# Optimization experiments

Hardware: AMD Instinct MI355X
Metric: run time of the kernel (lower is better)

Reference implementation:

```python
import jax, jax.numpy as jnp
import numpy as np

B, S = 1, 128            # batch, timesteps
N_LGN = 17400            # LGN input units (dense_shape[1])
N_POST = 50000           # V1 neurons (dense_shape[0])
NNZ = 800000             # number of synapses
N_BASIS = 5              # synaptic receptor basis functions
N_RECEPT = 10            # receptor types


def setup_inputs() -> dict:
    key = jax.random.key(0)
    k1, k2, k3, k4, k5, k6 = jax.random.split(key, 6)
    inp = jax.random.normal(k1, (B, S, N_LGN), dtype=jnp.float32)
    rows = jax.random.randint(k2, (NNZ,), 0, N_POST)
    cols = jax.random.randint(k3, (NNZ,), 0, N_LGN)
    indices = jnp.stack([rows, cols], axis=1)  # [nnz, 2] sparse coords
    weights = jax.random.normal(k4, (NNZ,), dtype=jnp.float32)
    synaptic_weights = jax.random.uniform(k5, (N_RECEPT, N_BASIS), dtype=jnp.float32)
    syn_ids = jax.random.randint(k6, (NNZ,), 0, N_RECEPT)
    return {
        "inp": inp,
        "indices": indices,
        "weights": weights,
        "synaptic_weights": synaptic_weights,
        "syn_ids": syn_ids,
        "n_neurons": N_POST,
    }


def reference(inp, indices, weights, synaptic_weights, syn_ids, n_neurons):
    b, s, n_lgn = inp.shape
    x = inp.reshape(b * s, n_lgn)               # [Bt, n_lgn], Bt = batch*time
    rows = indices[:, 0]                        # post-synaptic neuron id
    cols = indices[:, 1]                        # pre-synaptic LGN id
    factors = synaptic_weights[syn_ids]         # [nnz, n_basis] (tf.gather)
    xg = x.T[cols]                              # [nnz, Bt] gathered presyn activity
    n_basis = factors.shape[1]
    outs = []
    for r in range(n_basis):                    # small fixed loop over receptor bases
        vals = weights * factors[:, r]          # per-receptor sparse values
        # sparse_dense_matmul(sparse_w_in, inp, adjoint_b=True) == scatter-add over rows
        outs.append(jax.ops.segment_sum(xg * vals[:, None], rows, num_segments=n_neurons))
    i_in = jnp.stack(outs)                      # [n_basis, n_post, Bt]
    out = jnp.transpose(i_in, (2, 1, 0))        # [Bt, n_post, n_basis]
    return out.reshape(b, s, -1)                # [batch, time, n_post*n_basis]
```

## Files before the change

kernel.cpp:

```cpp
#include <hip/hip_runtime.h>
#include <hip/hip_bf16.h>
#include <stdint.h>

#define N_LGN   17400
#define N_POST  50000
#define NNZ     800000
#define N_BASIS 5
#define ELL_CAP 48

#define NBKT      196
#define CAPB      5120
#define BIN_CHUNK 4096
#define BIN_BLOCKS ((NNZ + BIN_CHUNK - 1) / BIN_CHUNK)

#define TPOSE_CBLK   32
#define TPOSE_BLOCKS ((N_LGN + TPOSE_CBLK - 1) / TPOSE_CBLK)

__global__ __launch_bounds__(256) void k_prep(const float* __restrict__ inp,
                                              __hip_bfloat162* __restrict__ xTb,
                                              const int2* __restrict__ idx2,
                                              const float* __restrict__ w,
                                              const int* __restrict__ syn,
                                              int* __restrict__ bucketCnt,
                                              int2* __restrict__ bEdges) {
    __shared__ alignas(16) int2 ebuf[BIN_CHUNK];
    __shared__ unsigned char sbuf[BIN_CHUNK];
    __shared__ int hcnt[256], hstart[256], hcur[256], gbase[256];
    int tid = threadIdx.x;
    if (blockIdx.x < BIN_BLOCKS) {
        int base = blockIdx.x * BIN_CHUNK;
        int ne = NNZ - base; if (ne > BIN_CHUNK) ne = BIN_CHUNK;
        hcnt[tid] = 0;
        __syncthreads();
        int2 pk[16]; int bk[16];
#pragma unroll
        for (int i = 0; i < 16; ++i) {
            int p = i * 256 + tid;
            bk[i] = -1;
            if (p < ne) {
                int2 rc = idx2[base + p];
                float wv = w[base + p];
                int sy = syn[base + p];
                int b  = rc.x >> 8;
                int rl = rc.x & 255;
                pk[i] = make_int2(rc.y | (sy << 15) | (rl << 19), __float_as_int(wv));
                bk[i] = b;
                atomicAdd(&hcnt[b], 1);
            }
        }
        __syncthreads();
        int v = hcnt[tid];
        hstart[tid] = v;
        __syncthreads();
        for (int off = 1; off < 256; off <<= 1) {
            int t = (tid >= off) ? hstart[tid - off] : 0;
            __syncthreads();
            hstart[tid] += t;
            __syncthreads();
        }
        int excl = hstart[tid] - v;
        hstart[tid] = excl;
        hcur[tid]  = excl;
        if (tid < NBKT) gbase[tid] = atomicAdd(&bucketCnt[tid], v);
        __syncthreads();
#pragma unroll
        for (int i = 0; i < 16; ++i) {
            if (bk[i] >= 0) {
                int pos = atomicAdd(&hcur[bk[i]], 1);
                ebuf[pos] = pk[i];
                sbuf[pos] = (unsigned char)bk[i];
            }
        }
        __syncthreads();
        for (int p = tid; p < ne; p += 256) {
            int b  = sbuf[p];
            int gi = gbase[b] + (p - hstart[b]);
            if (gi < CAPB) bEdges[b * CAPB + gi] = ebuf[p];
        }
    } else {
        float* tile = (float*)ebuf;
        int c0 = (blockIdx.x - BIN_BLOCKS) * TPOSE_CBLK;
        for (int it = 0; it < 16; ++it) {
            int flat = it * 256 + tid;
            int s  = flat >> 5;
            int cl = flat & 31;
            int c  = c0 + cl;
            float v = 0.0f;
            if (c < N_LGN) v = inp[s * N_LGN + c];
            tile[cl * 129 + s] = v;
        }
        __syncthreads();
        for (int it = 0; it < 8; ++it) {
            int flat = it * 256 + tid;
            int cl = flat >> 6;
            int sp = flat & 63;
            int c  = c0 + cl;
            if (c < N_LGN) {
                float2 f = make_float2(tile[cl * 129 + 2 * sp], tile[cl * 129 + 2 * sp + 1]);
                xTb[c * 64 + sp] = __float22bfloat162_rn(f);
            }
        }
    }
}

__global__ __launch_bounds__(512) void k_build(const int2* __restrict__ bEdges,
                                               const int* __restrict__ bucketCnt,
                                               int2* __restrict__ ell,
                                               int* __restrict__ counts) {
    __shared__ alignas(16) int2 slab[256 * ELL_CAP];
    __shared__ int rcnt[256];
    int tid = threadIdx.x;
    int b   = blockIdx.x;
    if (tid < 256) rcnt[tid] = 0;
    __syncthreads();
    int cnt = bucketCnt[b]; if (cnt > CAPB) cnt = CAPB;
    for (int p = tid; p < cnt; p += 512) {
        int2 e = bEdges[b * CAPB + p];
        int rl = (e.x >> 19) & 0xFF;
        int r = atomicAdd(&rcnt[rl], 1);
        if (r < ELL_CAP)
            slab[rl * ELL_CAP + r] =
                make_int2((e.x & 0x7FFF) | (((e.x >> 15) & 0xF) << 16), e.y);
    }
    __syncthreads();
    const int4* s4 = (const int4*)slab;
    int4* e4 = (int4*)(ell + (size_t)b * (256 * ELL_CAP));
    for (int i = tid; i < 256 * ELL_CAP / 2; i += 512) e4[i] = s4[i];
    if (tid < 256) {
        int row = b * 256 + tid;
        if (row < N_POST) counts[row] = rcnt[tid];
    }
}

__global__ __launch_bounds__(256) void k_transpose_bf16(const float* __restrict__ inp,
                                                        __hip_bfloat162* __restrict__ xTb) {
    __shared__ float tile[64 * 129];
    int c0  = blockIdx.x * 64;
    int tid = threadIdx.x;
    for (int it = 0; it < 32; ++it) {
        int flat = it * 256 + tid;
        int s  = flat >> 6;
        int cl = flat & 63;
        int c  = c0 + cl;
        float v = 0.0f;
        if (c < N_LGN) v = inp[s * N_LGN + c];
        tile[cl * 129 + s] = v;
    }
    __syncthreads();
    for (int it = 0; it < 16; ++it) {
        int flat = it * 256 + tid;
        int cl = flat >> 6;
        int sp = flat & 63;
        int c  = c0 + cl;
        if (c < N_LGN) {
            float2 f = make_float2(tile[cl * 129 + 2 * sp], tile[cl * 129 + 2 * sp + 1]);
            xTb[c * 64 + sp] = __float22bfloat162_rn(f);
        }
    }
}

__global__ __launch_bounds__(256) void k_hist(const int4* __restrict__ idx2,
                                              int* __restrict__ counts) {
    int t = blockIdx.x * 256 + threadIdx.x;
    if (t >= NNZ / 2) return;
    int4 rc = idx2[t];
    atomicAdd(&counts[rc.x], 1);
    atomicAdd(&counts[rc.z], 1);
}

__global__ __launch_bounds__(1024) void k_scan1(const int* __restrict__ counts,
                                                int* __restrict__ rowStart,
                                                int* __restrict__ blockSums) {
    __shared__ int tmp[1024];
    int tid = threadIdx.x;
    int gid = blockIdx.x * 1024 + tid;
    int v = (gid < N_POST) ? counts[gid] : 0;
    tmp[tid] = v;
    __syncthreads();
    for (int off = 1; off < 1024; off <<= 1) {
        int t = (tid >= off) ? tmp[tid - off] : 0;
        __syncthreads();
        tmp[tid] += t;
        __syncthreads();
    }
    if (gid < N_POST) rowStart[gid] = tmp[tid] - v;
    if (tid == 1023) blockSums[blockIdx.x] = tmp[1023];
}

__global__ __launch_bounds__(64) void k_scan2(const int* __restrict__ blockSums,
                                              int* __restrict__ blockOffsets, int nblk) {
    __shared__ int tmp[64];
    int tid = threadIdx.x;
    int v = (tid < nblk) ? blockSums[tid] : 0;
    tmp[tid] = v;
    __syncthreads();
    for (int off = 1; off < 64; off <<= 1) {
        int t = (tid >= off) ? tmp[tid - off] : 0;
        __syncthreads();
        tmp[tid] += t;
        __syncthreads();
    }
    if (tid < nblk) blockOffsets[tid] = tmp[tid] - v;
}

__global__ __launch_bounds__(1024) void k_scan3(int* __restrict__ rowStart,
                                                const int* __restrict__ blockOffsets) {
    int gid = blockIdx.x * 1024 + threadIdx.x;
    if (gid < N_POST) rowStart[gid] += blockOffsets[blockIdx.x];
}

__global__ __launch_bounds__(256) void k_scatter_csr(const int4* __restrict__ idx2,
                                                     const float2* __restrict__ w2,
                                                     const int2* __restrict__ syn2,
                                                     const int* __restrict__ rowStart,
                                                     int* __restrict__ cursor,
                                                     int2* __restrict__ edges) {
    int t = blockIdx.x * 256 + threadIdx.x;
    if (t >= NNZ / 2) return;
    int4 rc = idx2[t];
    float2 ww = w2[t];
    int2 sy = syn2[t];
    int p0 = rowStart[rc.x] + atomicAdd(&cursor[rc.x], 1);
    edges[p0] = make_int2(rc.y | (sy.x << 16), __float_as_int(ww.x));
    int p1 = rowStart[rc.z] + atomicAdd(&cursor[rc.z], 1);
    edges[p1] = make_int2(rc.w | (sy.y << 16), __float_as_int(ww.y));
}

#define EDGE_FMA(XW, FA, F4)                                          \
    a0[0] = fmaf((XW).x, (FA).x, a0[0]); a1[0] = fmaf((XW).y, (FA).x, a1[0]); \
    a0[1] = fmaf((XW).x, (FA).y, a0[1]); a1[1] = fmaf((XW).y, (FA).y, a1[1]); \
    a0[2] = fmaf((XW).x, (FA).z, a0[2]); a1[2] = fmaf((XW).y, (FA).z, a1[2]); \
    a0[3] = fmaf((XW).x, (FA).w, a0[3]); a1[3] = fmaf((XW).y, (FA).w, a1[3]); \
    a0[4] = fmaf((XW).x, (F4),   a0[4]); a1[4] = fmaf((XW).y, (F4),   a1[4]);

__global__ __launch_bounds__(512, 8) void k_compute(const __hip_bfloat162* __restrict__ xTb,
                                                    const int2* __restrict__ edges,
                                                    const int* __restrict__ rowStart,
                                                    const int* __restrict__ counts,
                                                    const float* __restrict__ sw,
                                                    float2* __restrict__ out2,
                                                    int cap, int useEll) {
    __shared__ alignas(16) float facsP[80];
    __shared__ float accLds[40 * 133];
    __shared__ alignas(16) int2 eLds[8 * ELL_CAP];
    int tid  = threadIdx.x;
    int wave = tid >> 6;
    int lane = tid & 63;
    int n    = blockIdx.x * 8 + wave;
    int cnt  = counts[n];
    if (cnt > cap) cnt = cap;

    if (tid < 50) facsP[(tid / 5) * 8 + (tid % 5)] = sw[tid];
    if (useEll && tid < 8 * ELL_CAP / 2) {
        ((int4*)eLds)[tid] =
            ((const int4*)(edges + (size_t)blockIdx.x * (8 * ELL_CAP)))[tid];
    }
    __syncthreads();

    float a0[N_BASIS] = {0.f, 0.f, 0.f, 0.f, 0.f};
    float a1[N_BASIS] = {0.f, 0.f, 0.f, 0.f, 0.f};

    if (useEll) {
        const int4* ep4 = (const int4*)(eLds + wave * ELL_CAP);
        int j = 0;
        for (; j + 3 < cnt; j += 4) {
            int4 E0 = ep4[(j >> 1)];
            int4 E1 = ep4[(j >> 1) + 1];
            int c0 = E0.x & 0xFFFF, sy0 = E0.x >> 16; float w0 = __int_as_float(E0.y);
            int c1 = E0.z & 0xFFFF, sy1 = E0.z >> 16; float w1 = __int_as_float(E0.w);
            int c2 = E1.x & 0xFFFF, sy2 = E1.x >> 16; float w2 = __int_as_float(E1.y);
            int c3 = E1.z & 0xFFFF, sy3 = E1.z >> 16; float w3 = __int_as_float(E1.w);
            float2 x0 = __bfloat1622float2(xTb[c0 * 64 + lane]);
            float2 x1 = __bfloat1622float2(xTb[c1 * 64 + lane]);
            float2 x2 = __bfloat1622float2(xTb[c2 * 64 + lane]);
            float2 x3 = __bfloat1622float2(xTb[c3 * 64 + lane]);
            float4 fA0 = *(const float4*)&facsP[sy0 * 8]; float f40 = facsP[sy0 * 8 + 4];
            float4 fA1 = *(const float4*)&facsP[sy1 * 8]; float f41 = facsP[sy1 * 8 + 4];
            float4 fA2 = *(const float4*)&facsP[sy2 * 8]; float f42 = facsP[sy2 * 8 + 4];
            float4 fA3 = *(const float4*)&facsP[sy3 * 8]; float f43 = facsP[sy3 * 8 + 4];
            float2 xw0 = make_float2(x0.x * w0, x0.y * w0);
            float2 xw1 = make_float2(x1.x * w1, x1.y * w1);
            float2 xw2 = make_float2(x2.x * w2, x2.y * w2);
            float2 xw3 = make_float2(x3.x * w3, x3.y * w3);
            EDGE_FMA(xw0, fA0, f40)
            EDGE_FMA(xw1, fA1, f41)
            EDGE_FMA(xw2, fA2, f42)
            EDGE_FMA(xw3, fA3, f43)
        }
        for (; j < cnt; ++j) {
            int2 e = eLds[wave * ELL_CAP + j];
            int c = e.x & 0xFFFF, sy = e.x >> 16;
            float w = __int_as_float(e.y);
            float2 x = __bfloat1622float2(xTb[c * 64 + lane]);
            float4 fA = *(const float4*)&facsP[sy * 8]; float f4 = facsP[sy * 8 + 4];
            float2 xw = make_float2(x.x * w, x.y * w);
            EDGE_FMA(xw, fA, f4)
        }
    } else {
        const int2* ep = edges + rowStart[n];
        int j = 0;
        for (; j + 1 < cnt; j += 2) {
            int2 e0 = ep[j];
            int2 e1 = ep[j + 1];
            int c0 = e0.x & 0xFFFF, sy0 = e0.x >> 16;
            int c1 = e1.x & 0xFFFF, sy1 = e1.x >> 16;
            float2 x0 = __bfloat1622float2(xTb[c0 * 64 + lane]);
            float2 x1 = __bfloat1622float2(xTb[c1 * 64 + lane]);
            float w0 = __int_as_float(e0.y);
            float w1 = __int_as_float(e1.y);
            float4 fA0 = *(const float4*)&facsP[sy0 * 8]; float f40 = facsP[sy0 * 8 + 4];
            float4 fA1 = *(const float4*)&facsP[sy1 * 8]; float f41 = facsP[sy1 * 8 + 4];
            float2 xw0 = make_float2(x0.x * w0, x0.y * w0);
            float2 xw1 = make_float2(x1.x * w1, x1.y * w1);
            EDGE_FMA(xw0, fA0, f40)
            EDGE_FMA(xw1, fA1, f41)
        }
        if (j < cnt) {
            int2 e0 = ep[j];
            int c0 = e0.x & 0xFFFF, sy0 = e0.x >> 16;
            float2 x0 = __bfloat1622float2(xTb[c0 * 64 + lane]);
            float w0 = __int_as_float(e0.y);
            float4 fA0 = *(const float4*)&facsP[sy0 * 8]; float f40 = facsP[sy0 * 8 + 4];
            float2 xw0 = make_float2(x0.x * w0, x0.y * w0);
            EDGE_FMA(xw0, fA0, f40)
        }
    }

#pragma unroll
    for (int r = 0; r < N_BASIS; ++r) {
        int jj = wave * 5 + r;
        accLds[jj * 133 + 2 * lane]     = a0[r];
        accLds[jj * 133 + 2 * lane + 1] = a1[r];
    }
    __syncthreads();

    int base2 = blockIdx.x * 20;
    for (int it = 0; it < 5; ++it) {
        int flat = it * 512 + tid;
        int s  = flat / 20;
        int jj = flat % 20;
        float f0 = accLds[(2 * jj) * 133 + s];
        float f1 = accLds[(2 * jj + 1) * 133 + s];
        out2[s * 125000 + base2 + jj] = make_float2(f0, f1);
    }
}

extern "C" void kernel_launch(void* const* d_in, const int* in_sizes, int n_in,
                              void* d_out, int out_size, void* d_ws, size_t ws_size,
                              hipStream_t stream) {
    const float* inp     = (const float*)d_in[0];
    const int*   indices = (const int*)d_in[1];
    const float* weights = (const float*)d_in[2];
    const float* sw      = (const float*)d_in[3];
    const int*   syn     = (const int*)d_in[4];

    char* ws = (char*)d_ws;
    __hip_bfloat162* xTb = (__hip_bfloat162*)(ws);
    int* counts          = (int*)(ws + 4454400);

    const size_t ELL_BYTES_END = 4654400ULL + (size_t)N_POST * ELL_CAP * 8;
    bool useEll = (ws_size >= ELL_BYTES_END);

    if (useEll) {
        int2* ell = (int2*)(ws + 4654400);
        int2* bEdges   = (int2*)d_out;
        int*  bucketCnt = (int*)((char*)d_out + (size_t)NBKT * CAPB * 8);
        hipMemsetAsync(bucketCnt, 0, 1024, stream);
        k_prep<<<BIN_BLOCKS + TPOSE_BLOCKS, 256, 0, stream>>>(
            inp, xTb, (const int2*)indices, weights, syn, bucketCnt, bEdges);
        k_build<<<NBKT, 512, 0, stream>>>(bEdges, bucketCnt, ell, counts);
        k_compute<<<N_POST / 8, 512, 0, stream>>>(xTb, ell, nullptr, counts, sw,
                                                  (float2*)d_out, ELL_CAP, 1);
    } else {
        int* cursor    = (int*)(ws + 4654400);
        int* rowStart  = (int*)(ws + 4854400);
        int* blockSums = (int*)(ws + 5054400);
        int* blockOffs = (int*)(ws + 5054656);
        int2* edges    = (int2*)(ws + 5054912);
        hipMemsetAsync(counts, 0, 400000, stream);
        k_transpose_bf16<<<(N_LGN + 63) / 64, 256, 0, stream>>>(inp, xTb);
        k_hist<<<(NNZ / 2 + 255) / 256, 256, 0, stream>>>((const int4*)indices, counts);
        k_scan1<<<(N_POST + 1023) / 1024, 1024, 0, stream>>>(counts, rowStart, blockSums);
        k_scan2<<<1, 64, 0, stream>>>(blockSums, blockOffs, (N_POST + 1023) / 1024);
        k_scan3<<<(N_POST + 1023) / 1024, 1024, 0, stream>>>(rowStart, blockOffs);
        k_scatter_csr<<<(NNZ / 2 + 255) / 256, 256, 0, stream>>>(
            (const int4*)indices, (const float2*)weights, (const int2*)syn,
            rowStart, cursor, edges);
        k_compute<<<N_POST / 8, 512, 0, stream>>>(xTb, edges, rowStart, counts, sw,
                                                  (float2*)d_out, 1 << 30, 0);
    }
}
```

Before: 214.7 us.

## Process two ELL rows per wave with zero-padded slabs to remove tail loops

Adds a dedicated ELL compute kernel in which each wave handles two neurons and walks both rows together in steps of four. Eight independent gathers are in flight per iteration instead of four. The build kernel now zero-fills the ELL slab, so padded entries contribute zero and the per-row tail loop can be dropped; iterations run to the longer of the two rows. The cost is more registers (launch bounds lowered to 6), extra work on padding entries, and an extra LDS zeroing pass in the build kernel.

Measured after the change: 205.8 us. 4.1% less time.

```diff
diff --git a/kernel.cpp b/kernel.cpp
--- a/kernel.cpp
+++ b/kernel.cpp
@@ -112,6 +112,10 @@
     int tid = threadIdx.x;
     int b   = blockIdx.x;
     if (tid < 256) rcnt[tid] = 0;
+    {
+        int4* s4w = (int4*)slab;
+        for (int i = tid; i < 256 * ELL_CAP / 2; i += 512) s4w[i] = make_int4(0, 0, 0, 0);
+    }
     __syncthreads();
     int cnt = bucketCnt[b]; if (cnt > CAPB) cnt = CAPB;
     for (int p = tid; p < cnt; p += 512) {
@@ -226,104 +230,147 @@
     edges[p1] = make_int2(rc.w | (sy.y << 16), __float_as_int(ww.y));
 }
 
-#define EDGE_FMA(XW, FA, F4)                                          \
-    a0[0] = fmaf((XW).x, (FA).x, a0[0]); a1[0] = fmaf((XW).y, (FA).x, a1[0]); \
-    a0[1] = fmaf((XW).x, (FA).y, a0[1]); a1[1] = fmaf((XW).y, (FA).y, a1[1]); \
-    a0[2] = fmaf((XW).x, (FA).z, a0[2]); a1[2] = fmaf((XW).y, (FA).z, a1[2]); \
-    a0[3] = fmaf((XW).x, (FA).w, a0[3]); a1[3] = fmaf((XW).y, (FA).w, a1[3]); \
-    a0[4] = fmaf((XW).x, (F4),   a0[4]); a1[4] = fmaf((XW).y, (F4),   a1[4]);
+#define EDGE_FMA2(P0, P1, XW, FA, F4)                                             \
+    P0[0] = fmaf((XW).x, (FA).x, P0[0]); P1[0] = fmaf((XW).y, (FA).x, P1[0]);     \
+    P0[1] = fmaf((XW).x, (FA).y, P0[1]); P1[1] = fmaf((XW).y, (FA).y, P1[1]);     \
+    P0[2] = fmaf((XW).x, (FA).z, P0[2]); P1[2] = fmaf((XW).y, (FA).z, P1[2]);     \
+    P0[3] = fmaf((XW).x, (FA).w, P0[3]); P1[3] = fmaf((XW).y, (FA).w, P1[3]);     \
+    P0[4] = fmaf((XW).x, (F4),   P0[4]); P1[4] = fmaf((XW).y, (F4),   P1[4]);
+
+#define DECODE_GATHER(EX, EY, XW, FA, F4)                                         \
+    {                                                                             \
+        int c_  = (EX) & 0xFFFF; int sy_ = (EX) >> 16;                            \
+        float2 x_ = __bfloat1622float2(xTb[c_ * 64 + lane]);                      \
+        float w_  = __int_as_float(EY);                                           \
+        FA = *(const float4*)&facsP[sy_ * 8]; F4 = facsP[sy_ * 8 + 4];            \
+        XW = make_float2(x_.x * w_, x_.y * w_);                                   \
+    }
+
+__global__ __launch_bounds__(512, 6) void k_compute_ell(const __hip_bfloat162* __restrict__ xTb,
+                                                        const int2* __restrict__ ell,
+                                                        const int* __restrict__ counts,
+                                                        const float* __restrict__ sw,
+                                                        float2* __restrict__ out2) {
+    __shared__ alignas(16) float facsP[80];
+    __shared__ float accLds[40 * 133];
+    __shared__ alignas(16) int2 eLds[16 * ELL_CAP];
+    int tid  = threadIdx.x;
+    int wave = tid >> 6;
+    int lane = tid & 63;
+    int n0   = blockIdx.x * 16;
+
+    if (tid < 50) facsP[(tid / 5) * 8 + (tid % 5)] = sw[tid];
+    if (tid < 16 * ELL_CAP / 2)
+        ((int4*)eLds)[tid] = ((const int4*)(ell + (size_t)n0 * ELL_CAP))[tid];
+    int cA = counts[n0 + wave];     if (cA > ELL_CAP) cA = ELL_CAP;
+    int cB = counts[n0 + 8 + wave]; if (cB > ELL_CAP) cB = ELL_CAP;
+    __syncthreads();
+
+    float aA0[N_BASIS] = {0.f, 0.f, 0.f, 0.f, 0.f};
+    float aA1[N_BASIS] = {0.f, 0.f, 0.f, 0.f, 0.f};
+    float aB0[N_BASIS] = {0.f, 0.f, 0.f, 0.f, 0.f};
+    float aB1[N_BASIS] = {0.f, 0.f, 0.f, 0.f, 0.f};
+
+    const int4* epA = (const int4*)(eLds + wave * ELL_CAP);
+    const int4* epB = (const int4*)(eLds + (wave + 8) * ELL_CAP);
+    int mc = cA > cB ? cA : cB;
+    for (int j = 0; j < mc; j += 4) {
+        int h = j >> 1;
+        int4 A0 = epA[h], A1 = epA[h + 1];
+        int4 B0 = epB[h], B1 = epB[h + 1];
+        float2 xwA0, xwA1, xwA2, xwA3, xwB0, xwB1, xwB2, xwB3;
+        float4 fAA0, fAA1, fAA2, fAA3, fAB0, fAB1, fAB2, fAB3;
+        float  f4A0, f4A1, f4A2, f4A3, f4B0, f4B1, f4B2, f4B3;
+        DECODE_GATHER(A0.x, A0.y, xwA0, fAA0, f4A0)
+        DECODE_GATHER(A0.z, A0.w, xwA1, fAA1, f4A1)
+        DECODE_GATHER(A1.x, A1.y, xwA2, fAA2, f4A2)
+        DECODE_GATHER(A1.z, A1.w, xwA3, fAA3, f4A3)
+        DECODE_GATHER(B0.x, B0.y, xwB0, fAB0, f4B0)
+        DECODE_GATHER(B0.z, B0.w, xwB1, fAB1, f4B1)
+        DECODE_GATHER(B1.x, B1.y, xwB2, fAB2, f4B2)
+        DECODE_GATHER(B1.z, B1.w, xwB3, fAB3, f4B3)
+        EDGE_FMA2(aA0, aA1, xwA0, fAA0, f4A0)
+        EDGE_FMA2(aA0, aA1, xwA1, fAA1, f4A1)
+        EDGE_FMA2(aA0, aA1, xwA2, fAA2, f4A2)
+        EDGE_FMA2(aA0, aA1, xwA3, fAA3, f4A3)
+        EDGE_FMA2(aB0, aB1, xwB0, fAB0, f4B0)
+        EDGE_FMA2(aB0, aB1, xwB1, fAB1, f4B1)
+        EDGE_FMA2(aB0, aB1, xwB2, fAB2, f4B2)
+        EDGE_FMA2(aB0, aB1, xwB3, fAB3, f4B3)
+    }
+
+    int base2 = blockIdx.x * 40;
+#pragma unroll
+    for (int r = 0; r < N_BASIS; ++r) {
+        int jj = wave * 5 + r;
+        accLds[jj * 133 + 2 * lane]     = aA0[r];
+        accLds[jj * 133 + 2 * lane + 1] = aA1[r];
+    }
+    __syncthreads();
+    for (int it = 0; it < 5; ++it) {
+        int flat = it * 512 + tid;
+        int s  = flat / 20;
+        int jj = flat % 20;
+        float f0 = accLds[(2 * jj) * 133 + s];
+        float f1 = accLds[(2 * jj + 1) * 133 + s];
+        out2[s * 125000 + base2 + jj] = make_float2(f0, f1);
+    }
+    __syncthreads();
+#pragma unroll
+    for (int r = 0; r < N_BASIS; ++r) {
+        int jj = wave * 5 + r;
+        accLds[jj * 133 + 2 * lane]     = aB0[r];
+        accLds[jj * 133 + 2 * lane + 1] = aB1[r];
+    }
+    __syncthreads();
+    for (int it = 0; it < 5; ++it) {
+        int flat = it * 512 + tid;
+        int s  = flat / 20;
+        int jj = flat % 20;
+        float f0 = accLds[(2 * jj) * 133 + s];
+        float f1 = accLds[(2 * jj + 1) * 133 + s];
+        out2[s * 125000 + base2 + 20 + jj] = make_float2(f0, f1);
+    }
+}
+
+#define EDGE_FMA(XW, FA, F4) EDGE_FMA2(a0, a1, XW, FA, F4)
 
 __global__ __launch_bounds__(512, 8) void k_compute(const __hip_bfloat162* __restrict__ xTb,
                                                     const int2* __restrict__ edges,
                                                     const int* __restrict__ rowStart,
                                                     const int* __restrict__ counts,
                                                     const float* __restrict__ sw,
-                                                    float2* __restrict__ out2,
-                                                    int cap, int useEll) {
+                                                    float2* __restrict__ out2) {
     __shared__ alignas(16) float facsP[80];
     __shared__ float accLds[40 * 133];
-    __shared__ alignas(16) int2 eLds[8 * ELL_CAP];
     int tid  = threadIdx.x;
     int wave = tid >> 6;
     int lane = tid & 63;
     int n    = blockIdx.x * 8 + wave;
     int cnt  = counts[n];
-    if (cnt > cap) cnt = cap;
 
     if (tid < 50) facsP[(tid / 5) * 8 + (tid % 5)] = sw[tid];
-    if (useEll && tid < 8 * ELL_CAP / 2) {
-        ((int4*)eLds)[tid] =
-            ((const int4*)(edges + (size_t)blockIdx.x * (8 * ELL_CAP)))[tid];
-    }
     __syncthreads();
 
     float a0[N_BASIS] = {0.f, 0.f, 0.f, 0.f, 0.f};
     float a1[N_BASIS] = {0.f, 0.f, 0.f, 0.f, 0.f};
 
-    if (useEll) {
-        const int4* ep4 = (const int4*)(eLds + wave * ELL_CAP);
-        int j = 0;
-        for (; j + 3 < cnt; j += 4) {
-            int4 E0 = ep4[(j >> 1)];
-            int4 E1 = ep4[(j >> 1) + 1];
-            int c0 = E0.x & 0xFFFF, sy0 = E0.x >> 16; float w0 = __int_as_float(E0.y);
-            int c1 = E0.z & 0xFFFF, sy1 = E0.z >> 16; float w1 = __int_as_float(E0.w);
-            int c2 = E1.x & 0xFFFF, sy2 = E1.x >> 16; float w2 = __int_as_float(E1.y);
-            int c3 = E1.z & 0xFFFF, sy3 = E1.z >> 16; float w3 = __int_as_float(E1.w);
-            float2 x0 = __bfloat1622float2(xTb[c0 * 64 + lane]);
-            float2 x1 = __bfloat1622float2(xTb[c1 * 64 + lane]);
-            float2 x2 = __bfloat1622float2(xTb[c2 * 64 + lane]);
-            float2 x3 = __bfloat1622float2(xTb[c3 * 64 + lane]);
-            float4 fA0 = *(const float4*)&facsP[sy0 * 8]; float f40 = facsP[sy0 * 8 + 4];
-            float4 fA1 = *(const float4*)&facsP[sy1 * 8]; float f41 = facsP[sy1 * 8 + 4];
-            float4 fA2 = *(const float4*)&facsP[sy2 * 8]; float f42 = facsP[sy2 * 8 + 4];
-            float4 fA3 = *(const float4*)&facsP[sy3 * 8]; float f43 = facsP[sy3 * 8 + 4];
-            float2 xw0 = make_float2(x0.x * w0, x0.y * w0);
-            float2 xw1 = make_float2(x1.x * w1, x1.y * w1);
-            float2 xw2 = make_float2(x2.x * w2, x2.y * w2);
-            float2 xw3 = make_float2(x3.x * w3, x3.y * w3);
-            EDGE_FMA(xw0, fA0, f40)
-            EDGE_FMA(xw1, fA1, f41)
-            EDGE_FMA(xw2, fA2, f42)
-            EDGE_FMA(xw3, fA3, f43)
-        }
-        for (; j < cnt; ++j) {
-            int2 e = eLds[wave * ELL_CAP + j];
-            int c = e.x & 0xFFFF, sy = e.x >> 16;
-            float w = __int_as_float(e.y);
-            float2 x = __bfloat1622float2(xTb[c * 64 + lane]);
-            float4 fA = *(const float4*)&facsP[sy * 8]; float f4 = facsP[sy * 8 + 4];
-            float2 xw = make_float2(x.x * w, x.y * w);
-            EDGE_FMA(xw, fA, f4)
-        }
-    } else {
-        const int2* ep = edges + rowStart[n];
-        int j = 0;
-        for (; j + 1 < cnt; j += 2) {
-            int2 e0 = ep[j];
-            int2 e1 = ep[j + 1];
-            int c0 = e0.x & 0xFFFF, sy0 = e0.x >> 16;
-            int c1 = e1.x & 0xFFFF, sy1 = e1.x >> 16;
-            float2 x0 = __bfloat1622float2(xTb[c0 * 64 + lane]);
-            float2 x1 = __bfloat1622float2(xTb[c1 * 64 + lane]);
-            float w0 = __int_as_float(e0.y);
-            float w1 = __int_as_float(e1.y);
-            float4 fA0 = *(const float4*)&facsP[sy0 * 8]; float f40 = facsP[sy0 * 8 + 4];
-            float4 fA1 = *(const float4*)&facsP[sy1 * 8]; float f41 = facsP[sy1 * 8 + 4];
-            float2 xw0 = make_float2(x0.x * w0, x0.y * w0);
-            float2 xw1 = make_float2(x1.x * w1, x1.y * w1);
-            EDGE_FMA(xw0, fA0, f40)
-            EDGE_FMA(xw1, fA1, f41)
-        }
-        if (j < cnt) {
-            int2 e0 = ep[j];
-            int c0 = e0.x & 0xFFFF, sy0 = e0.x >> 16;
-            float2 x0 = __bfloat1622float2(xTb[c0 * 64 + lane]);
-            float w0 = __int_as_float(e0.y);
-            float4 fA0 = *(const float4*)&facsP[sy0 * 8]; float f40 = facsP[sy0 * 8 + 4];
-            float2 xw0 = make_float2(x0.x * w0, x0.y * w0);
-            EDGE_FMA(xw0, fA0, f40)
-        }
+    const int2* ep = edges + rowStart[n];
+    int j = 0;
+    for (; j + 1 < cnt; j += 2) {
+        int2 e0 = ep[j];
+        int2 e1 = ep[j + 1];
+        float2 xw0, xw1; float4 fA0, fA1; float f40, f41;
+        DECODE_GATHER(e0.x, e0.y, xw0, fA0, f40)
+        DECODE_GATHER(e1.x, e1.y, xw1, fA1, f41)
+        EDGE_FMA(xw0, fA0, f40)
+        EDGE_FMA(xw1, fA1, f41)
+    }
+    if (j < cnt) {
+        int2 e0 = ep[j];
+        float2 xw0; float4 fA0; float f40;
+        DECODE_GATHER(e0.x, e0.y, xw0, fA0, f40)
+        EDGE_FMA(xw0, fA0, f40)
     }
 
 #pragma unroll
@@ -369,8 +416,8 @@
         k_prep<<<BIN_BLOCKS + TPOSE_BLOCKS, 256, 0, stream>>>(
             inp, xTb, (const int2*)indices, weights, syn, bucketCnt, bEdges);
         k_build<<<NBKT, 512, 0, stream>>>(bEdges, bucketCnt, ell, counts);
-        k_compute<<<N_POST / 8, 512, 0, stream>>>(xTb, ell, nullptr, counts, sw,
-                                                  (float2*)d_out, ELL_CAP, 1);
+        k_compute_ell<<<N_POST / 16, 512, 0, stream>>>(xTb, ell, counts, sw,
+                                                       (float2*)d_out);
     } else {
         int* cursor    = (int*)(ws + 4654400);
         int* rowStart  = (int*)(ws + 4854400);
@@ -387,6 +434,6 @@
             (const int4*)indices, (const float2*)weights, (const int2*)syn,
             rowStart, cursor, edges);
         k_compute<<<N_POST / 8, 512, 0, stream>>>(xTb, edges, rowStart, counts, sw,
-                                                  (float2*)d_out, 1 << 30, 0);
-    }
-}
+                                                  (float2*)d_out);
+    }
+}
```
